# Performance work log

Hardware: AMD Instinct MI355X
Metric: run time of the kernel (lower is better)

## Reference

```python
import jax, jax.numpy as jnp
import numpy as np

N_NODES = 131072
N_EDGES = 2097152
IN_DIM = 256
HID = 128
BATCH = 32
MAX_COM = 10
C = 1.0          # Poincare ball curvature
EPS = 1e-5
MIN_NORM = 1e-15


def _row_norm(x):
    return jnp.sqrt(jnp.clip(jnp.sum(x * x, axis=-1, keepdims=True), MIN_NORM, None))


def proj(x, c=C):
    # clip points inside the Poincare ball of radius (1-eps)/sqrt(c)
    norm = _row_norm(x)
    maxnorm = (1.0 - EPS) / jnp.sqrt(c)
    return jnp.where(norm > maxnorm, x / norm * maxnorm, x)


def logmap0(x, c=C):
    sqrt_c = jnp.sqrt(c)
    norm = _row_norm(x)
    arg = jnp.clip(sqrt_c * norm, None, 1.0 - 1e-7)
    return x * jnp.arctanh(arg) / (sqrt_c * norm)


def expmap0(u, c=C):
    sqrt_c = jnp.sqrt(c)
    norm = _row_norm(u)
    return u * jnp.tanh(sqrt_c * norm) / (sqrt_c * norm)


def gcn_layer(x, W, b, src, dst, n_nodes):
    # support = x @ W ; out[dst] += support[src] ; out += b  (raw adjacency spmm)
    support = x @ W
    agg = jax.ops.segment_sum(support[src], dst, num_segments=n_nodes)
    return agg + b


def setup_inputs() -> dict:
    key = jax.random.key(0)
    ks = jax.random.split(key, 8)
    x = jax.random.normal(ks[0], (N_NODES, IN_DIM), dtype=jnp.float32) * 0.1
    src = jax.random.randint(ks[1], (N_EDGES,), 0, N_NODES)
    dst = jax.random.randint(ks[2], (N_EDGES,), 0, N_NODES)
    seg_ids = jax.random.randint(ks[3], (N_NODES,), 0, BATCH * MAX_COM)
    W1 = jax.random.normal(ks[4], (IN_DIM, HID), dtype=jnp.float32) / np.sqrt(IN_DIM)
    b1 = jnp.zeros((HID,), dtype=jnp.float32)
    W2 = jax.random.normal(ks[5], (HID, HID), dtype=jnp.float32) / np.sqrt(HID)
    b2 = jnp.zeros((HID,), dtype=jnp.float32)
    return {"x": x, "src": src, "dst": dst, "seg_ids": seg_ids,
            "W1": W1, "b1": b1, "W2": W2, "b2": b2,
            "batch_size": BATCH, "max_comments": MAX_COM}


def reference(x, src, dst, seg_ids, W1, b1, W2, b2, batch_size, max_comments):
    n_nodes = x.shape[0]
    h = jnp.tanh(gcn_layer(x, W1, b1, src, dst, n_nodes))
    h = jnp.tanh(gcn_layer(h, W2, b2, src, dst, n_nodes))
    # tangent-space coordinates
    h = logmap0(proj(h))
    # per-(batch, comment) subgraph mean pooling == segment mean
    n_seg = batch_size * max_comments
    sums = jax.ops.segment_sum(h, seg_ids, num_segments=n_seg)
    counts = jax.ops.segment_sum(jnp.ones((n_nodes,), h.dtype), seg_ids, num_segments=n_seg)
    agg = sums / jnp.maximum(counts, 1.0)[:, None]   # empty segments -> zeros (padding)
    agg = proj(expmap0(agg))
    return agg.reshape(batch_size, max_comments, -1)
```

## Files before the change

kernel.cpp:

```cpp
#include <hip/hip_runtime.h>
#include <hip/hip_bf16.h>

#define IN_DIM 256
#define HID    128
#define NSEG   320
#define MAXNORM 0.99999

typedef short bf16x8 __attribute__((ext_vector_type(8)));
typedef float f32x4  __attribute__((ext_vector_type(4)));

static __device__ __forceinline__ ushort f2b(float f) {
    uint u = __builtin_bit_cast(uint, f);
    uint r = 0x7FFFu + ((u >> 16) & 1u);
    return (ushort)((u + r) >> 16);
}
static __device__ __forceinline__ float b2f_lo(uint v) {
    return __builtin_bit_cast(float, v << 16);
}
static __device__ __forceinline__ float b2f_hi(uint v) {
    return __builtin_bit_cast(float, v & 0xFFFF0000u);
}

__global__ void count_edges_k(const int* __restrict__ dst, int* __restrict__ counts, int n) {
    int e = blockIdx.x * 256 + threadIdx.x;
    if (e < n) atomicAdd(&counts[dst[e]], 1);
}

__global__ void scan_block_k(const int* __restrict__ in, int* __restrict__ out,
                             int* __restrict__ partials) {
    __shared__ int sh[256];
    int tid = threadIdx.x;
    int base = blockIdx.x * 1024 + tid * 4;
    int4 v = *(const int4*)&in[base];
    int s = v.x + v.y + v.z + v.w;
    sh[tid] = s;
    __syncthreads();
#pragma unroll
    for (int off = 1; off < 256; off <<= 1) {
        int t = (tid >= off) ? sh[tid - off] : 0;
        __syncthreads();
        sh[tid] += t;
        __syncthreads();
    }
    int excl = sh[tid] - s;
    int4 o;
    o.x = excl; o.y = excl + v.x; o.z = o.y + v.y; o.w = o.z + v.z;
    *(int4*)&out[base] = o;
    if (tid == 255) partials[blockIdx.x] = sh[255];
}

__global__ void scan_partials_k(int* __restrict__ partials, int n) {
    __shared__ int sh[1024];
    int tid = threadIdx.x;
    int v = (tid < n) ? partials[tid] : 0;
    sh[tid] = v;
    __syncthreads();
    for (int off = 1; off < blockDim.x; off <<= 1) {
        int t = (tid >= off) ? sh[tid - off] : 0;
        __syncthreads();
        sh[tid] += t;
        __syncthreads();
    }
    if (tid < n) partials[tid] = sh[tid] - v;
}

__global__ void add_base_k(int* __restrict__ offsets, const int* __restrict__ partials, int n) {
    int g = blockIdx.x * 256 + threadIdx.x;
    if (g < n) offsets[g] += partials[g >> 10];
}

__global__ void fill_edges_k(const int* __restrict__ src, const int* __restrict__ dst,
                             const int* __restrict__ offsets, int* __restrict__ cursor,
                             int* __restrict__ sorted_src, int n) {
    int e = blockIdx.x * 256 + threadIdx.x;
    if (e < n) {
        int d = dst[e];
        int pos = atomicAdd(&cursor[d], 1);
        sorted_src[offsets[d] + pos] = src[e];
    }
}

__global__ void prep_wt_k(const float* __restrict__ w1, const float* __restrict__ w2,
                          ushort* __restrict__ w1t, ushort* __restrict__ w2t) {
    int id = blockIdx.x * 256 + threadIdx.x;
    if (id < 32768) {
        int n = id >> 8, k = id & 255;
        w1t[n * 256 + k] = f2b(w1[k * 128 + n]);
    } else {
        int id2 = id - 32768;
        int n = id2 >> 7, k = id2 & 127;
        w2t[n * 128 + k] = f2b(w2[k * 128 + n]);
    }
}

template<bool AF32>
__global__ __launch_bounds__(256) void gemm_k(const void* __restrict__ Ap,
                                              const ushort* __restrict__ BT,
                                              ushort* __restrict__ C, int K) {
    __shared__ __align__(16) char As[16384];
    __shared__ __align__(16) char Bs[16384];
    const int tid = threadIdx.x;
    const int lane = tid & 63;
    const int wid = tid >> 6;
    const int wr = wid >> 1, wc = wid & 1;
    const int row0 = blockIdx.x * 128;
    f32x4 acc[4][4] = {};

    for (int k0 = 0; k0 < K; k0 += 64) {
        if (AF32) {
            const float* A = (const float*)Ap;
#pragma unroll
            for (int it = 0; it < 8; ++it) {
                int id = tid + it * 256;
                int r = id >> 4, c4 = (id & 15) * 4;
                float4 v = *(const float4*)&A[(size_t)(row0 + r) * K + k0 + c4];
                ushort4 h;
                h.x = f2b(v.x); h.y = f2b(v.y); h.z = f2b(v.z); h.w = f2b(v.w);
                *(ushort4*)(As + ((r * 128 + c4 * 2) ^ ((r & 7) << 4))) = h;
            }
        } else {
            const ushort* A = (const ushort*)Ap;
#pragma unroll
            for (int it = 0; it < 4; ++it) {
                int id = tid + it * 256;
                int r = id >> 3, c8 = (id & 7) * 8;
                bf16x8 v = *(const bf16x8*)&A[(size_t)(row0 + r) * K + k0 + c8];
                *(bf16x8*)(As + ((r * 128 + c8 * 2) ^ ((r & 7) << 4))) = v;
            }
        }
#pragma unroll
        for (int it = 0; it < 4; ++it) {
            int id = tid + it * 256;
            int n = id >> 3, c8 = (id & 7) * 8;
            bf16x8 v = *(const bf16x8*)&BT[(size_t)n * K + k0 + c8];
            *(bf16x8*)(Bs + ((n * 128 + c8 * 2) ^ ((n & 7) << 4))) = v;
        }
        __syncthreads();
#pragma unroll
        for (int kc = 0; kc < 2; ++kc) {
            bf16x8 af[4], bfr[4];
            int kb = (kc * 32 + (lane >> 4) * 8) * 2;
#pragma unroll
            for (int i = 0; i < 4; ++i) {
                int r = wr * 64 + i * 16 + (lane & 15);
                af[i] = *(const bf16x8*)(As + ((r * 128 + kb) ^ ((r & 7) << 4)));
                int n = wc * 64 + i * 16 + (lane & 15);
                bfr[i] = *(const bf16x8*)(Bs + ((n * 128 + kb) ^ ((n & 7) << 4)));
            }
#pragma unroll
            for (int i = 0; i < 4; ++i)
#pragma unroll
                for (int j = 0; j < 4; ++j)
                    acc[i][j] = __builtin_amdgcn_mfma_f32_16x16x32_bf16(
                        af[i], bfr[j], acc[i][j], 0, 0, 0);
        }
        __syncthreads();
    }
#pragma unroll
    for (int i = 0; i < 4; ++i)
#pragma unroll
        for (int j = 0; j < 4; ++j)
#pragma unroll
            for (int r = 0; r < 4; ++r) {
                int row = row0 + wr * 64 + i * 16 + (lane >> 4) * 4 + r;
                int col = wc * 64 + j * 16 + (lane & 15);
                C[(size_t)row * 128 + col] = f2b(acc[i][j][r]);
            }
}

static __device__ __forceinline__ void gather_node(
    const uint* __restrict__ sup, const int* __restrict__ offsets,
    const int* __restrict__ counts, const int* __restrict__ ssrc,
    const float* __restrict__ bias, int node, int lane, float& ax, float& ay) {
    node = __builtin_amdgcn_readfirstlane(node);
    int off = __builtin_amdgcn_readfirstlane(offsets[node]);
    int cnt = __builtin_amdgcn_readfirstlane(counts[node]);
    float2 bv = *(const float2*)&bias[2 * lane];
    ax = bv.x;
    ay = bv.y;
    int j = 0;
    for (; j + 16 <= cnt; j += 16) {
        uint v[16];
#pragma unroll
        for (int t = 0; t < 16; ++t) {
            int s = ssrc[off + j + t];
            v[t] = sup[(size_t)s * 64 + lane];
        }
#pragma unroll
        for (int t = 0; t < 16; ++t) { ax += b2f_lo(v[t]); ay += b2f_hi(v[t]); }
    }
    for (; j + 4 <= cnt; j += 4) {
        uint v[4];
#pragma unroll
        for (int t = 0; t < 4; ++t) {
            int s = ssrc[off + j + t];
            v[t] = sup[(size_t)s * 64 + lane];
        }
#pragma unroll
        for (int t = 0; t < 4; ++t) { ax += b2f_lo(v[t]); ay += b2f_hi(v[t]); }
    }
    for (; j < cnt; ++j) {
        int s = ssrc[off + j];
        uint v = sup[(size_t)s * 64 + lane];
        ax += b2f_lo(v); ay += b2f_hi(v);
    }
}

__global__ __launch_bounds__(256) void gather_tanh_k(
    const uint* __restrict__ sup, const int* __restrict__ offsets,
    const int* __restrict__ counts, const int* __restrict__ ssrc,
    const float* __restrict__ bias, uint* __restrict__ h1, int n_nodes) {
    int node = (blockIdx.x << 2) | (threadIdx.x >> 6);
    if (node >= n_nodes) return;
    int lane = threadIdx.x & 63;
    float ax, ay;
    gather_node(sup, offsets, counts, ssrc, bias, node, lane, ax, ay);
    uint o = ((uint)f2b(tanhf(ay)) << 16) | (uint)f2b(tanhf(ax));
    h1[(size_t)node * 64 + lane] = o;
}

__global__ __launch_bounds__(256) void gather_pool_k(
    const uint* __restrict__ sup, const int* __restrict__ offsets,
    const int* __restrict__ counts, const int* __restrict__ ssrc,
    const float* __restrict__ bias, const int* __restrict__ seg_ids,
    float* __restrict__ sums, int* __restrict__ seg_cnt, int n_nodes) {
    int node = (blockIdx.x << 2) | (threadIdx.x >> 6);
    if (node >= n_nodes) return;
    int lane = threadIdx.x & 63;
    float ax, ay;
    gather_node(sup, offsets, counts, ssrc, bias, node, lane, ax, ay);
    float hx = tanhf(ax), hy = tanhf(ay);
    float ss = hx * hx + hy * hy;
#pragma unroll
    for (int o = 32; o > 0; o >>= 1) ss += __shfl_xor(ss, o);
    double r = sqrt((double)fmaxf(ss, 1e-15f));
    double m = fmin(r, MAXNORM);
    float f = (float)(atanh(m) / r);
    int seg = seg_ids[node];
    atomicAdd(&sums[seg * 128 + 2 * lane], hx * f);
    atomicAdd(&sums[seg * 128 + 2 * lane + 1], hy * f);
    if (lane == 0) atomicAdd(&seg_cnt[seg], 1);
}

__global__ __launch_bounds__(64) void finalize_k(const float* __restrict__ sums,
                                                 const int* __restrict__ seg_cnt,
                                                 float* __restrict__ out) {
    int seg = blockIdx.x;
    int lane = threadIdx.x;
    float c = fmaxf((float)seg_cnt[seg], 1.0f);
    float ux = sums[seg * 128 + 2 * lane] / c;
    float uy = sums[seg * 128 + 2 * lane + 1] / c;
    float ss = ux * ux + uy * uy;
#pragma unroll
    for (int o = 32; o > 0; o >>= 1) ss += __shfl_xor(ss, o);
    double r = sqrt((double)fmaxf(ss, 1e-15f));
    double t = tanh(r);
    double fac = t / r;
    if (t > MAXNORM) fac = MAXNORM / r;
    float f = (float)fac;
    out[seg * 128 + 2 * lane] = ux * f;
    out[seg * 128 + 2 * lane + 1] = uy * f;
}

extern "C" void kernel_launch(void* const* d_in, const int* in_sizes, int n_in,
                              void* d_out, int out_size, void* d_ws, size_t ws_size,
                              hipStream_t stream) {
    const float* x   = (const float*)d_in[0];
    const int* src   = (const int*)d_in[1];
    const int* dst   = (const int*)d_in[2];
    const int* segid = (const int*)d_in[3];
    const float* W1  = (const float*)d_in[4];
    const float* b1  = (const float*)d_in[5];
    const float* W2  = (const float*)d_in[6];
    const float* b2  = (const float*)d_in[7];
    float* out       = (float*)d_out;

    const int N = in_sizes[3];
    const int E = in_sizes[1];

    char* ws = (char*)d_ws;
    ushort* supA   = (ushort*)(ws);
    uint*   supA32 = (uint*)supA;
    ushort* h1     = (ushort*)(ws + 33554432);
    uint*   h1u    = (uint*)h1;
    int* ssrc      = (int*)(ws + 67108864);
    int* counts    = (int*)(ws + 75497472);
    int* offsets   = (int*)(ws + 76021760);
    int* cursor    = (int*)(ws + 76546048);
    int* partials  = (int*)(ws + 77070336);
    float* sums    = (float*)(ws + 77071360);
    int* seg_cnt   = (int*)(ws + 77235200);
    ushort* w1t    = (ushort*)(ws + 77236480);
    ushort* w2t    = (ushort*)(ws + 77302016);

    hipMemsetAsync(counts, 0, (size_t)N * 4, stream);
    hipMemsetAsync(cursor, 0, (size_t)N * 4, stream);
    hipMemsetAsync(sums, 0, (size_t)NSEG * 128 * 4, stream);
    hipMemsetAsync(seg_cnt, 0, (size_t)NSEG * 4, stream);

    const int eblocks = (E + 255) / 256;
    const int nscan = N / 1024;

    prep_wt_k<<<192, 256, 0, stream>>>(W1, W2, w1t, w2t);

    count_edges_k<<<eblocks, 256, 0, stream>>>(dst, counts, E);
    scan_block_k<<<nscan, 256, 0, stream>>>(counts, offsets, partials);
    scan_partials_k<<<1, nscan, 0, stream>>>(partials, nscan);
    add_base_k<<<(N + 255) / 256, 256, 0, stream>>>(offsets, partials, N);
    fill_edges_k<<<eblocks, 256, 0, stream>>>(src, dst, offsets, cursor, ssrc, E);

    gemm_k<true><<<N / 128, 256, 0, stream>>>(x, w1t, supA, IN_DIM);
    gather_tanh_k<<<N / 4, 256, 0, stream>>>(supA32, offsets, counts, ssrc, b1, h1u, N);

    gemm_k<false><<<N / 128, 256, 0, stream>>>(h1, w2t, supA, HID);
    gather_pool_k<<<N / 4, 256, 0, stream>>>(supA32, offsets, counts, ssrc, b2, segid,
                                             sums, seg_cnt, N);

    finalize_k<<<NSEG, 64, 0, stream>>>(sums, seg_cnt, out);
}
```

Before: 594.4 us.

## Bucket edges by destination group and source panel for locality-aware gathering

Edges are now sorted by a composite key of an 8-node destination group and a source-ID panel, and packed with the local destination index. Each wave handles whole groups, accumulating 8 nodes in LDS, so gathers within a group walk source rows in panel order. The aim is better L2 locality for the random sup reads and fewer per-node setup costs. The trade-offs are a larger counting/scan over 512K keys and LDS read-modify-write traffic on every edge.

```diff
diff --git a/kernel.cpp b/kernel.cpp
--- a/kernel.cpp
+++ b/kernel.cpp
@@ -6,6 +6,12 @@
 #define NSEG   320
 #define MAXNORM 0.99999
 
+#define G      8
+#define NGRP   16384
+#define NPAN   32
+#define PANSH  12
+#define NKEY   (NGRP * NPAN)
+
 typedef short bf16x8 __attribute__((ext_vector_type(8)));
 typedef float f32x4  __attribute__((ext_vector_type(4)));
 
@@ -21,9 +27,13 @@
     return __builtin_bit_cast(float, v & 0xFFFF0000u);
 }
 
-__global__ void count_edges_k(const int* __restrict__ dst, int* __restrict__ counts, int n) {
+__global__ void count_edges_k(const int* __restrict__ src, const int* __restrict__ dst,
+                              int* __restrict__ counts, int n) {
     int e = blockIdx.x * 256 + threadIdx.x;
-    if (e < n) atomicAdd(&counts[dst[e]], 1);
+    if (e < n) {
+        int key = ((dst[e] >> 3) << 5) | (src[e] >> PANSH);
+        atomicAdd(&counts[key], 1);
+    }
 }
 
 __global__ void scan_block_k(const int* __restrict__ in, int* __restrict__ out,
@@ -71,13 +81,20 @@
 
 __global__ void fill_edges_k(const int* __restrict__ src, const int* __restrict__ dst,
                              const int* __restrict__ offsets, int* __restrict__ cursor,
-                             int* __restrict__ sorted_src, int n) {
+                             uint* __restrict__ packed, int n) {
     int e = blockIdx.x * 256 + threadIdx.x;
     if (e < n) {
-        int d = dst[e];
-        int pos = atomicAdd(&cursor[d], 1);
-        sorted_src[offsets[d] + pos] = src[e];
-    }
+        int s = src[e], d = dst[e];
+        int key = ((d >> 3) << 5) | (s >> PANSH);
+        int pos = atomicAdd(&cursor[key], 1);
+        packed[offsets[key] + pos] = (uint)s | ((uint)(d & 7) << 28);
+    }
+}
+
+__global__ void extract_goff_k(const int* __restrict__ offsets, int* __restrict__ goff, int E) {
+    int g = blockIdx.x * 256 + threadIdx.x;
+    if (g < NGRP) goff[g] = offsets[g << 5];
+    if (g == NGRP) goff[g] = E;
 }
 
 __global__ void prep_wt_k(const float* __restrict__ w1, const float* __restrict__ w2,
@@ -168,78 +185,82 @@
             }
 }
 
-static __device__ __forceinline__ void gather_node(
-    const uint* __restrict__ sup, const int* __restrict__ offsets,
-    const int* __restrict__ counts, const int* __restrict__ ssrc,
-    const float* __restrict__ bias, int node, int lane, float& ax, float& ay) {
-    node = __builtin_amdgcn_readfirstlane(node);
-    int off = __builtin_amdgcn_readfirstlane(offsets[node]);
-    int cnt = __builtin_amdgcn_readfirstlane(counts[node]);
+template<bool POOL>
+__global__ __launch_bounds__(256, 8) void gather_grp_k(
+    const uint* __restrict__ sup, const int* __restrict__ goff,
+    const uint* __restrict__ packed, const float* __restrict__ bias,
+    const int* __restrict__ seg_ids, uint* __restrict__ h1,
+    float* __restrict__ sums, int* __restrict__ seg_cnt) {
+    __shared__ float lds[4][G * 128];
+    const int wslot = threadIdx.x >> 6;
+    const int lane  = threadIdx.x & 63;
+    float* acc = &lds[wslot][0];
+    const int wave = blockIdx.x * 4 + wslot;
     float2 bv = *(const float2*)&bias[2 * lane];
-    ax = bv.x;
-    ay = bv.y;
-    int j = 0;
-    for (; j + 16 <= cnt; j += 16) {
-        uint v[16];
-#pragma unroll
-        for (int t = 0; t < 16; ++t) {
-            int s = ssrc[off + j + t];
-            v[t] = sup[(size_t)s * 64 + lane];
-        }
-#pragma unroll
-        for (int t = 0; t < 16; ++t) { ax += b2f_lo(v[t]); ay += b2f_hi(v[t]); }
-    }
-    for (; j + 4 <= cnt; j += 4) {
-        uint v[4];
-#pragma unroll
-        for (int t = 0; t < 4; ++t) {
-            int s = ssrc[off + j + t];
-            v[t] = sup[(size_t)s * 64 + lane];
-        }
-#pragma unroll
-        for (int t = 0; t < 4; ++t) { ax += b2f_lo(v[t]); ay += b2f_hi(v[t]); }
-    }
-    for (; j < cnt; ++j) {
-        int s = ssrc[off + j];
-        uint v = sup[(size_t)s * 64 + lane];
-        ax += b2f_lo(v); ay += b2f_hi(v);
-    }
-}
-
-__global__ __launch_bounds__(256) void gather_tanh_k(
-    const uint* __restrict__ sup, const int* __restrict__ offsets,
-    const int* __restrict__ counts, const int* __restrict__ ssrc,
-    const float* __restrict__ bias, uint* __restrict__ h1, int n_nodes) {
-    int node = (blockIdx.x << 2) | (threadIdx.x >> 6);
-    if (node >= n_nodes) return;
-    int lane = threadIdx.x & 63;
-    float ax, ay;
-    gather_node(sup, offsets, counts, ssrc, bias, node, lane, ax, ay);
-    uint o = ((uint)f2b(tanhf(ay)) << 16) | (uint)f2b(tanhf(ax));
-    h1[(size_t)node * 64 + lane] = o;
-}
-
-__global__ __launch_bounds__(256) void gather_pool_k(
-    const uint* __restrict__ sup, const int* __restrict__ offsets,
-    const int* __restrict__ counts, const int* __restrict__ ssrc,
-    const float* __restrict__ bias, const int* __restrict__ seg_ids,
-    float* __restrict__ sums, int* __restrict__ seg_cnt, int n_nodes) {
-    int node = (blockIdx.x << 2) | (threadIdx.x >> 6);
-    if (node >= n_nodes) return;
-    int lane = threadIdx.x & 63;
-    float ax, ay;
-    gather_node(sup, offsets, counts, ssrc, bias, node, lane, ax, ay);
-    float hx = tanhf(ax), hy = tanhf(ay);
-    float ss = hx * hx + hy * hy;
-#pragma unroll
-    for (int o = 32; o > 0; o >>= 1) ss += __shfl_xor(ss, o);
-    double r = sqrt((double)fmaxf(ss, 1e-15f));
-    double m = fmin(r, MAXNORM);
-    float f = (float)(atanh(m) / r);
-    int seg = seg_ids[node];
-    atomicAdd(&sums[seg * 128 + 2 * lane], hx * f);
-    atomicAdd(&sums[seg * 128 + 2 * lane + 1], hy * f);
-    if (lane == 0) atomicAdd(&seg_cnt[seg], 1);
+
+    for (int sweep = 0; sweep < 2; ++sweep) {
+        const int g = wave * 2 + sweep;
+#pragma unroll
+        for (int n = 0; n < G; ++n)
+            *(float2*)&acc[n * 128 + 2 * lane] = float2{0.f, 0.f};
+
+        int base = goff[g];
+        int cnt  = goff[g + 1] - base;
+        int j = 0;
+        while (j < cnt) {
+            int rem = cnt - j; if (rem > 64) rem = 64;
+            uint pe = 0;
+            if (lane < rem) pe = packed[base + j + lane];
+            int t = 0;
+            for (; t + 16 <= rem; t += 16) {
+                uint r[16];
+#pragma unroll
+                for (int u = 0; u < 16; ++u) {
+                    uint p = __builtin_amdgcn_readlane(pe, t + u);
+                    uint s = p & 0xFFFFFFu;
+                    r[u] = sup[(size_t)s * 64 + lane];
+                }
+#pragma unroll
+                for (int u = 0; u < 16; ++u) {
+                    uint p = __builtin_amdgcn_readlane(pe, t + u);
+                    uint l = p >> 28;
+                    float2 a = *(float2*)&acc[l * 128 + 2 * lane];
+                    a.x += b2f_lo(r[u]); a.y += b2f_hi(r[u]);
+                    *(float2*)&acc[l * 128 + 2 * lane] = a;
+                }
+            }
+            for (; t < rem; ++t) {
+                uint p = __builtin_amdgcn_readlane(pe, t);
+                uint s = p & 0xFFFFFFu;
+                uint l = p >> 28;
+                uint v = sup[(size_t)s * 64 + lane];
+                float2 a = *(float2*)&acc[l * 128 + 2 * lane];
+                a.x += b2f_lo(v); a.y += b2f_hi(v);
+                *(float2*)&acc[l * 128 + 2 * lane] = a;
+            }
+            j += rem;
+        }
+#pragma unroll
+        for (int n = 0; n < G; ++n) {
+            int node = g * G + n;
+            float2 a = *(float2*)&acc[n * 128 + 2 * lane];
+            float hx = tanhf(a.x + bv.x), hy = tanhf(a.y + bv.y);
+            if (!POOL) {
+                h1[(size_t)node * 64 + lane] = ((uint)f2b(hy) << 16) | (uint)f2b(hx);
+            } else {
+                float ss = hx * hx + hy * hy;
+#pragma unroll
+                for (int o = 32; o > 0; o >>= 1) ss += __shfl_xor(ss, o);
+                double rr = sqrt((double)fmaxf(ss, 1e-15f));
+                double m = fmin(rr, MAXNORM);
+                float f = (float)(atanh(m) / rr);
+                int seg = seg_ids[node];
+                atomicAdd(&sums[seg * 128 + 2 * lane], hx * f);
+                atomicAdd(&sums[seg * 128 + 2 * lane + 1], hy * f);
+                if (lane == 0) atomicAdd(&seg_cnt[seg], 1);
+            }
+        }
+    }
 }
 
 __global__ __launch_bounds__(64) void finalize_k(const float* __restrict__ sums,
@@ -281,40 +302,42 @@
     char* ws = (char*)d_ws;
     ushort* supA   = (ushort*)(ws);
     uint*   supA32 = (uint*)supA;
-    ushort* h1     = (ushort*)(ws + 33554432);
-    uint*   h1u    = (uint*)h1;
-    int* ssrc      = (int*)(ws + 67108864);
-    int* counts    = (int*)(ws + 75497472);
-    int* offsets   = (int*)(ws + 76021760);
-    int* cursor    = (int*)(ws + 76546048);
-    int* partials  = (int*)(ws + 77070336);
-    float* sums    = (float*)(ws + 77071360);
-    int* seg_cnt   = (int*)(ws + 77235200);
-    ushort* w1t    = (ushort*)(ws + 77236480);
-    ushort* w2t    = (ushort*)(ws + 77302016);
-
-    hipMemsetAsync(counts, 0, (size_t)N * 4, stream);
-    hipMemsetAsync(cursor, 0, (size_t)N * 4, stream);
+    uint*   h1u    = (uint*)(ws + 33554432);
+    ushort* h1     = (ushort*)h1u;
+    uint* packed   = (uint*)(ws + 67108864);
+    int* goff      = (int*)(ws + 75497472);
+    float* sums    = (float*)(ws + 75563264);
+    int* seg_cnt   = (int*)(ws + 75727104);
+    ushort* w1t    = (ushort*)(ws + 75728384);
+    ushort* w2t    = (ushort*)(ws + 75793920);
+    int* counts    = (int*)(ws);
+    int* offsets   = (int*)(ws + 2097152);
+    int* cursor    = (int*)(ws + 4194304);
+    int* partials  = (int*)(ws + 6291456);
+
+    hipMemsetAsync(counts, 0, (size_t)NKEY * 4, stream);
+    hipMemsetAsync(cursor, 0, (size_t)NKEY * 4, stream);
     hipMemsetAsync(sums, 0, (size_t)NSEG * 128 * 4, stream);
     hipMemsetAsync(seg_cnt, 0, (size_t)NSEG * 4, stream);
 
     const int eblocks = (E + 255) / 256;
-    const int nscan = N / 1024;
 
     prep_wt_k<<<192, 256, 0, stream>>>(W1, W2, w1t, w2t);
 
-    count_edges_k<<<eblocks, 256, 0, stream>>>(dst, counts, E);
-    scan_block_k<<<nscan, 256, 0, stream>>>(counts, offsets, partials);
-    scan_partials_k<<<1, nscan, 0, stream>>>(partials, nscan);
-    add_base_k<<<(N + 255) / 256, 256, 0, stream>>>(offsets, partials, N);
-    fill_edges_k<<<eblocks, 256, 0, stream>>>(src, dst, offsets, cursor, ssrc, E);
+    count_edges_k<<<eblocks, 256, 0, stream>>>(src, dst, counts, E);
+    scan_block_k<<<NKEY / 1024, 256, 0, stream>>>(counts, offsets, partials);
+    scan_partials_k<<<1, NKEY / 1024, 0, stream>>>(partials, NKEY / 1024);
+    add_base_k<<<NKEY / 256, 256, 0, stream>>>(offsets, partials, NKEY);
+    fill_edges_k<<<eblocks, 256, 0, stream>>>(src, dst, offsets, cursor, packed, E);
+    extract_goff_k<<<(NGRP + 256) / 256, 256, 0, stream>>>(offsets, goff, E);
 
     gemm_k<true><<<N / 128, 256, 0, stream>>>(x, w1t, supA, IN_DIM);
-    gather_tanh_k<<<N / 4, 256, 0, stream>>>(supA32, offsets, counts, ssrc, b1, h1u, N);
+    gather_grp_k<false><<<2048, 256, 0, stream>>>(supA32, goff, packed, b1, segid,
+                                                  h1u, sums, seg_cnt);
 
     gemm_k<false><<<N / 128, 256, 0, stream>>>(h1, w2t, supA, HID);
-    gather_pool_k<<<N / 4, 256, 0, stream>>>(supA32, offsets, counts, ssrc, b2, segid,
-                                             sums, seg_cnt, N);
+    gather_grp_k<true><<<2048, 256, 0, stream>>>(supA32, goff, packed, b2, segid,
+                                                 h1u, sums, seg_cnt);
 
     finalize_k<<<NSEG, 64, 0, stream>>>(sums, seg_cnt, out);
 }
```

New measurement: 597.7 us. Within noise of the previous version (+0.6%).

## Gather four edges per wave with 16-byte loads and shuffle-broadcast indices

Applied to the files above, without the earlier changes.

Replaces the one-edge-per-wave gather, where each lane read 4 bytes of a row, with a scheme that splits the wave into four quarter-waves. Each quarter-wave reads a different neighbour row using 16-byte loads. Edge indices are loaded once per lane and broadcast with shuffles, and partial sums are combined across quarters with xor-shuffles. This is meant to raise memory-level parallelism and cut the number of load instructions. In exchange it adds shuffle overhead, handles edges beyond 64 serially on one quarter, and issues more atomics per lane in the pooling variant.

```diff
diff --git a/kernel.cpp b/kernel.cpp
--- a/kernel.cpp
+++ b/kernel.cpp
@@ -168,78 +168,96 @@
             }
 }
 
-static __device__ __forceinline__ void gather_node(
-    const uint* __restrict__ sup, const int* __restrict__ offsets,
-    const int* __restrict__ counts, const int* __restrict__ ssrc,
-    const float* __restrict__ bias, int node, int lane, float& ax, float& ay) {
-    node = __builtin_amdgcn_readfirstlane(node);
-    int off = __builtin_amdgcn_readfirstlane(offsets[node]);
-    int cnt = __builtin_amdgcn_readfirstlane(counts[node]);
-    float2 bv = *(const float2*)&bias[2 * lane];
-    ax = bv.x;
-    ay = bv.y;
-    int j = 0;
-    for (; j + 16 <= cnt; j += 16) {
-        uint v[16];
-#pragma unroll
-        for (int t = 0; t < 16; ++t) {
-            int s = ssrc[off + j + t];
-            v[t] = sup[(size_t)s * 64 + lane];
-        }
-#pragma unroll
-        for (int t = 0; t < 16; ++t) { ax += b2f_lo(v[t]); ay += b2f_hi(v[t]); }
-    }
-    for (; j + 4 <= cnt; j += 4) {
-        uint v[4];
-#pragma unroll
-        for (int t = 0; t < 4; ++t) {
-            int s = ssrc[off + j + t];
-            v[t] = sup[(size_t)s * 64 + lane];
-        }
-#pragma unroll
-        for (int t = 0; t < 4; ++t) { ax += b2f_lo(v[t]); ay += b2f_hi(v[t]); }
-    }
-    for (; j < cnt; ++j) {
-        int s = ssrc[off + j];
-        uint v = sup[(size_t)s * 64 + lane];
-        ax += b2f_lo(v); ay += b2f_hi(v);
-    }
-}
-
-__global__ __launch_bounds__(256) void gather_tanh_k(
-    const uint* __restrict__ sup, const int* __restrict__ offsets,
-    const int* __restrict__ counts, const int* __restrict__ ssrc,
-    const float* __restrict__ bias, uint* __restrict__ h1, int n_nodes) {
-    int node = (blockIdx.x << 2) | (threadIdx.x >> 6);
-    if (node >= n_nodes) return;
-    int lane = threadIdx.x & 63;
-    float ax, ay;
-    gather_node(sup, offsets, counts, ssrc, bias, node, lane, ax, ay);
-    uint o = ((uint)f2b(tanhf(ay)) << 16) | (uint)f2b(tanhf(ax));
-    h1[(size_t)node * 64 + lane] = o;
-}
-
-__global__ __launch_bounds__(256) void gather_pool_k(
-    const uint* __restrict__ sup, const int* __restrict__ offsets,
+#define ACC8(vv)                                                       \
+    do { acc[0] += b2f_lo((vv).x); acc[1] += b2f_hi((vv).x);           \
+         acc[2] += b2f_lo((vv).y); acc[3] += b2f_hi((vv).y);           \
+         acc[4] += b2f_lo((vv).z); acc[5] += b2f_hi((vv).z);           \
+         acc[6] += b2f_lo((vv).w); acc[7] += b2f_hi((vv).w); } while (0)
+
+template<bool POOL>
+__global__ __launch_bounds__(256) void gather_x4_k(
+    const ushort* __restrict__ sup, const int* __restrict__ offsets,
     const int* __restrict__ counts, const int* __restrict__ ssrc,
     const float* __restrict__ bias, const int* __restrict__ seg_ids,
-    float* __restrict__ sums, int* __restrict__ seg_cnt, int n_nodes) {
-    int node = (blockIdx.x << 2) | (threadIdx.x >> 6);
-    if (node >= n_nodes) return;
-    int lane = threadIdx.x & 63;
-    float ax, ay;
-    gather_node(sup, offsets, counts, ssrc, bias, node, lane, ax, ay);
-    float hx = tanhf(ax), hy = tanhf(ay);
-    float ss = hx * hx + hy * hy;
-#pragma unroll
-    for (int o = 32; o > 0; o >>= 1) ss += __shfl_xor(ss, o);
-    double r = sqrt((double)fmaxf(ss, 1e-15f));
-    double m = fmin(r, MAXNORM);
-    float f = (float)(atanh(m) / r);
-    int seg = seg_ids[node];
-    atomicAdd(&sums[seg * 128 + 2 * lane], hx * f);
-    atomicAdd(&sums[seg * 128 + 2 * lane + 1], hy * f);
-    if (lane == 0) atomicAdd(&seg_cnt[seg], 1);
+    uint* __restrict__ h1, float* __restrict__ sums, int* __restrict__ seg_cnt,
+    int n_nodes) {
+    const int node = (blockIdx.x << 2) | (threadIdx.x >> 6);
+    const int lane = threadIdx.x & 63;
+    const int q = lane >> 4, c = lane & 15;
+    const int off = offsets[node];
+    const int cnt = counts[node];
+    const int n0 = min(cnt, 64);
+    float acc[8] = {};
+    int my = 0;
+    if (lane < n0) my = ssrc[off + lane];
+
+    int j = 0;
+    for (; j + 16 <= n0; j += 16) {
+        uint4 v[4];
+#pragma unroll
+        for (int u = 0; u < 4; ++u) {
+            int r = __shfl(my, j + u * 4 + q);
+            v[u] = *(const uint4*)&sup[(size_t)r * 128 + c * 8];
+        }
+#pragma unroll
+        for (int u = 0; u < 4; ++u) ACC8(v[u]);
+    }
+    if (j < n0) {
+#pragma unroll
+        for (int u = 0; u < 4; ++u) {
+            int e = j + u * 4 + q;
+            int r = __shfl(my, e);
+            if (e < n0) {
+                uint4 v = *(const uint4*)&sup[(size_t)r * 128 + c * 8];
+                ACC8(v);
+            }
+        }
+    }
+    for (int e = 64; e < cnt; ++e) {
+        if (q == 0) {
+            int r = ssrc[off + e];
+            uint4 v = *(const uint4*)&sup[(size_t)r * 128 + c * 8];
+            ACC8(v);
+        }
+    }
+#pragma unroll
+    for (int i = 0; i < 8; ++i) {
+        acc[i] += __shfl_xor(acc[i], 16);
+        acc[i] += __shfl_xor(acc[i], 32);
+    }
+    float4 b0 = *(const float4*)&bias[c * 8];
+    float4 b1 = *(const float4*)&bias[c * 8 + 4];
+    float h[8];
+    h[0] = tanhf(acc[0] + b0.x); h[1] = tanhf(acc[1] + b0.y);
+    h[2] = tanhf(acc[2] + b0.z); h[3] = tanhf(acc[3] + b0.w);
+    h[4] = tanhf(acc[4] + b1.x); h[5] = tanhf(acc[5] + b1.y);
+    h[6] = tanhf(acc[6] + b1.z); h[7] = tanhf(acc[7] + b1.w);
+
+    if (!POOL) {
+        if (q == 0) {
+            uint4 o;
+            o.x = ((uint)f2b(h[1]) << 16) | (uint)f2b(h[0]);
+            o.y = ((uint)f2b(h[3]) << 16) | (uint)f2b(h[2]);
+            o.z = ((uint)f2b(h[5]) << 16) | (uint)f2b(h[4]);
+            o.w = ((uint)f2b(h[7]) << 16) | (uint)f2b(h[6]);
+            *(uint4*)&h1[(size_t)node * 64 + c * 4] = o;
+        }
+    } else {
+        float ss = h[0]*h[0] + h[1]*h[1] + h[2]*h[2] + h[3]*h[3]
+                 + h[4]*h[4] + h[5]*h[5] + h[6]*h[6] + h[7]*h[7];
+#pragma unroll
+        for (int o2 = 1; o2 <= 8; o2 <<= 1) ss += __shfl_xor(ss, o2);
+        double rr = sqrt((double)fmaxf(ss, 1e-15f));
+        double m = fmin(rr, MAXNORM);
+        float f = (float)(atanh(m) / rr);
+        if (q == 0) {
+            int seg = seg_ids[node];
+#pragma unroll
+            for (int i = 0; i < 8; ++i)
+                atomicAdd(&sums[seg * 128 + c * 8 + i], h[i] * f);
+            if (lane == 0) atomicAdd(&seg_cnt[seg], 1);
+        }
+    }
 }
 
 __global__ __launch_bounds__(64) void finalize_k(const float* __restrict__ sums,
@@ -280,9 +298,8 @@
 
     char* ws = (char*)d_ws;
     ushort* supA   = (ushort*)(ws);
-    uint*   supA32 = (uint*)supA;
-    ushort* h1     = (ushort*)(ws + 33554432);
-    uint*   h1u    = (uint*)h1;
+    uint*   h1u    = (uint*)(ws + 33554432);
+    ushort* h1     = (ushort*)h1u;
     int* ssrc      = (int*)(ws + 67108864);
     int* counts    = (int*)(ws + 75497472);
     int* offsets   = (int*)(ws + 76021760);
@@ -310,11 +327,12 @@
     fill_edges_k<<<eblocks, 256, 0, stream>>>(src, dst, offsets, cursor, ssrc, E);
 
     gemm_k<true><<<N / 128, 256, 0, stream>>>(x, w1t, supA, IN_DIM);
-    gather_tanh_k<<<N / 4, 256, 0, stream>>>(supA32, offsets, counts, ssrc, b1, h1u, N);
+    gather_x4_k<false><<<N / 4, 256, 0, stream>>>(supA, offsets, counts, ssrc, b1,
+                                                  segid, h1u, sums, seg_cnt, N);
 
     gemm_k<false><<<N / 128, 256, 0, stream>>>(h1, w2t, supA, HID);
-    gather_pool_k<<<N / 4, 256, 0, stream>>>(supA32, offsets, counts, ssrc, b2, segid,
-                                             sums, seg_cnt, N);
+    gather_x4_k<true><<<N / 4, 256, 0, stream>>>(supA, offsets, counts, ssrc, b2,
+                                                 segid, h1u, sums, seg_cnt, N);
 
     finalize_k<<<NSEG, 64, 0, stream>>>(sums, seg_cnt, out);
 }
```

After: 911.8 us. 53.4% more time.
